# Kernel tuning notes

Hardware: AMD Instinct MI355X
Metric: run time of the kernel (lower is better)

Reference implementation:

```python
import jax, jax.numpy as jnp
import numpy as np

INPUT_DIM = 1024
OUTPUT_DIM = 1024
DEGREE = 8
N_TOKENS = 8192


def setup_inputs() -> dict:
    key = jax.random.key(0)
    k1, k2 = jax.random.split(key)
    x = jax.random.normal(k1, (N_TOKENS, INPUT_DIM), dtype=jnp.float32)
    # xavier_normal_ with gain = 1/(input_dim*(degree+1)) over fan dims (output_dim, degree+1)
    fan_in, fan_out = OUTPUT_DIM, DEGREE + 1  # torch treats dim0/dim1 as fans; scale is tiny anyway
    gain = 1.0 / (INPUT_DIM * (DEGREE + 1))
    std = gain * np.sqrt(2.0 / (INPUT_DIM + OUTPUT_DIM))
    cheby_coeffs = std * jax.random.normal(k2, (INPUT_DIM, OUTPUT_DIM, DEGREE + 1), dtype=jnp.float32)
    return {"x": x, "cheby_coeffs": cheby_coeffs}


def reference(x, cheby_coeffs):
    # x: (..., input_dim) -> y: (..., output_dim)
    degree_p1 = cheby_coeffs.shape[-1]
    theta = jnp.arccos(jnp.tanh(x))                      # (..., i)
    arange = jnp.arange(degree_p1, dtype=x.dtype)        # (d,)
    basis = jnp.cos(theta[..., None] * arange)           # (..., i, d) Chebyshev T_d(tanh(x))
    y = jnp.einsum('...id,iod->...o', basis, cheby_coeffs)
    return y
```

## Files before the change

kernel.cpp:

```cpp
#include <hip/hip_runtime.h>


typedef __bf16 bf16;
typedef __bf16 bf16x8 __attribute__((ext_vector_type(8)));
typedef float f32x2 __attribute__((ext_vector_type(2)));
typedef float f32x4 __attribute__((ext_vector_type(4)));
typedef float f32x16 __attribute__((ext_vector_type(16)));

__device__ __forceinline__ float fast_tanh(float a) {
  float e = __expf(a + a);
  return 1.f - 2.f * __builtin_amdgcn_rcpf(e + 1.f);
}

__global__ __launch_bounds__(256)
void cheby_prep(const float* __restrict__ x, const float* __restrict__ C,
                bf16* __restrict__ Bt, float* __restrict__ bias_p,
                float* __restrict__ th) {
  const int bid = blockIdx.x, tid = threadIdx.x;
  if (bid >= 1024) {
    const int r = bid - 1024;
    f32x4 v = *(const f32x4*)(x + (size_t)r * 1024 + tid * 4);
    f32x4 t;
    #pragma unroll
    for (int j = 0; j < 4; ++j) t[j] = fast_tanh(v[j]);
    *(f32x2*)(th + (size_t)r * 1024 + tid * 2)       = (f32x2){t.x, t.z};
    *(f32x2*)(th + (size_t)r * 1024 + 512 + tid * 2) = (f32x2){t.y, t.w};
    return;
  }
  __shared__ float tile[32][292];
  const int i0 = (bid >> 5) * 32, o0 = (bid & 31) * 32;
  {
    const int r = tid >> 3, seg = tid & 7;
    const float* src = C + (size_t)(i0 + r) * 9216 + (size_t)o0 * 9 + seg * 36;
    float* dst = &tile[r][seg * 36];
    #pragma unroll
    for (int v = 0; v < 9; ++v) *(f32x4*)(dst + v * 4) = *(const f32x4*)(src + v * 4);
  }
  __syncthreads();
  #pragma unroll
  for (int j = 0; j < 4; ++j) {
    int e = tid + 256 * j;
    int il = e >> 5, ol = e & 31;
    int i = i0 + il, o = o0 + ol;
    bf16x8 v;
    #pragma unroll
    for (int d = 0; d < 8; ++d) v[d] = (bf16)tile[il][ol * 9 + 1 + d];
    size_t idx16 = ((size_t)((o >> 7) * 128 + (i >> 3)) * 8 + (i & 7)) * 128 + (o & 127);
    *(bf16x8*)&Bt[idx16 * 8] = v;
  }
  if (tid < 32) {
    float s = 0.f;
    #pragma unroll
    for (int i = 0; i < 32; ++i) s += tile[i][tid * 9];
    bias_p[(size_t)(bid >> 5) * 1024 + o0 + tid] = s;
  }
}

__global__ __launch_bounds__(256, 2)
void cheby_gemm(const float* __restrict__ th, const bf16* __restrict__ Bt,
                const float* __restrict__ bias_p, float* __restrict__ out) {
  const int tid  = threadIdx.x;
  const int lane = tid & 63, w = tid >> 6;
  const int ml = lane & 31, h = lane >> 5;
  const int nb = blockIdx.x & 7;
  const int mb = blockIdx.x >> 3;
  const int wn = w & 1, wm = w >> 1;
  const int t0 = mb * 128 + wm * 64;
  const int o0 = nb * 128 + wn * 64;

  const bf16* btl = Bt + (((size_t)nb * 1024 + h) * 128 + (size_t)wn * 64 + ml) * 8;
  const float* sp0 = th + (size_t)(t0 + ml) * 1024 + h * 512;
  const float* sp1 = sp0 + 32 * 1024;

  f32x16 acc[2][2];
  #pragma unroll
  for (int a = 0; a < 2; ++a)
    #pragma unroll
    for (int b = 0; b < 2; ++b)
      #pragma unroll
      for (int r = 0; r < 16; ++r) acc[a][b][r] = 0.f;

  f32x4  sa[4], sb[4];
  bf16x8 bfr[2][4][2];

  sa[0] = *(const f32x4*)(sp0);     sb[0] = *(const f32x4*)(sp1);
  sa[1] = *(const f32x4*)(sp0 + 4); sb[1] = *(const f32x4*)(sp1 + 4);
  #pragma unroll
  for (int ks = 0; ks < 4; ++ks) {
    bfr[0][ks][0] = *(const bf16x8*)(btl + ks * 2048);
    bfr[0][ks][1] = *(const bf16x8*)(btl + ks * 2048 + 256);
  }

  #pragma unroll 1
  for (int s4 = 0; s4 < 128; s4 += 4) {
    #pragma unroll
    for (int u = 0; u < 4; ++u) {
      const int s = s4 + u;
      {
        int sl = s + 2; if (sl > 127) sl = 127;
        sa[(u + 2) & 3] = *(const f32x4*)(sp0 + sl * 4);
        sb[(u + 2) & 3] = *(const f32x4*)(sp1 + sl * 4);
      }
      {
        int bl = s + 1; if (bl > 127) bl = 127;
        const bf16* g = btl + (size_t)bl * 8192;
        #pragma unroll
        for (int ks = 0; ks < 4; ++ks) {
          bfr[(u + 1) & 1][ks][0] = *(const bf16x8*)(g + ks * 2048);
          bfr[(u + 1) & 1][ks][1] = *(const bf16x8*)(g + ks * 2048 + 256);
        }
      }
      bf16x8 afr[2][4];
      #pragma unroll
      for (int r = 0; r < 2; ++r) {
        const f32x4 sd = r ? sb[u & 3] : sa[u & 3];
        #pragma unroll
        for (int ks = 0; ks < 4; ++ks) {
          const float t  = sd[ks];
          const float T2 = __builtin_fmaf(t + t, t, -1.f);
          const float c2 = T2 + T2;
          const f32x2 c2v = {c2, c2};
          f32x2 pm1 = {t, 1.f};
          f32x2 p   = {t, T2};
          #pragma unroll
          for (int j2 = 0; j2 < 4; ++j2) {
            afr[r][ks][2 * j2]     = (bf16)p.x;
            afr[r][ks][2 * j2 + 1] = (bf16)p.y;
            f32x2 pn = c2v * p - pm1;
            pm1 = p; p = pn;
          }
        }
      }
      #pragma unroll
      for (int ks = 0; ks < 4; ++ks) {
        acc[0][0] = __builtin_amdgcn_mfma_f32_32x32x16_bf16(afr[0][ks], bfr[u & 1][ks][0], acc[0][0], 0, 0, 0);
        acc[0][1] = __builtin_amdgcn_mfma_f32_32x32x16_bf16(afr[0][ks], bfr[u & 1][ks][1], acc[0][1], 0, 0, 0);
        acc[1][0] = __builtin_amdgcn_mfma_f32_32x32x16_bf16(afr[1][ks], bfr[u & 1][ks][0], acc[1][0], 0, 0, 0);
        acc[1][1] = __builtin_amdgcn_mfma_f32_32x32x16_bf16(afr[1][ks], bfr[u & 1][ks][1], acc[1][1], 0, 0, 0);
      }
    }
  }

  float bv0 = 0.f, bv1 = 0.f;
  #pragma unroll
  for (int p = 0; p < 32; ++p) {
    bv0 += bias_p[(size_t)p * 1024 + o0 + ml];
    bv1 += bias_p[(size_t)p * 1024 + o0 + 32 + ml];
  }
  #pragma unroll
  for (int mt = 0; mt < 2; ++mt)
    #pragma unroll
    for (int r = 0; r < 16; ++r) {
      int row = t0 + mt * 32 + (r & 3) + 8 * (r >> 2) + 4 * h;
      float* po = out + (size_t)row * 1024 + o0 + ml;
      po[0]  = acc[mt][0][r] + bv0;
      po[32] = acc[mt][1][r] + bv1;
    }
}

__global__ __launch_bounds__(256)
void cheby_naive(const float* __restrict__ x, const float* __restrict__ C,
                 float* __restrict__ out) {
  const int t = blockIdx.x, tid = threadIdx.x;
  float acc[4] = {0.f, 0.f, 0.f, 0.f};
  for (int i = 0; i < 1024; ++i) {
    float th = tanhf(x[(size_t)t * 1024 + i]);
    float T[9]; T[0] = 1.f; T[1] = th;
    #pragma unroll
    for (int d = 2; d < 9; ++d) T[d] = 2.f * th * T[d - 1] - T[d - 2];
    #pragma unroll
    for (int j = 0; j < 4; ++j) {
      const float* cp = &C[((size_t)i * 1024 + tid + j * 256) * 9];
      float s = 0.f;
      #pragma unroll
      for (int d = 0; d < 9; ++d) s += T[d] * cp[d];
      acc[j] += s;
    }
  }
  #pragma unroll
  for (int j = 0; j < 4; ++j) out[(size_t)t * 1024 + tid + j * 256] = acc[j];
}

extern "C" void kernel_launch(void* const* d_in, const int* in_sizes, int n_in,
                              void* d_out, int out_size, void* d_ws, size_t ws_size,
                              hipStream_t stream) {
  (void)in_sizes; (void)n_in; (void)out_size;
  const float* x = (const float*)d_in[0];
  const float* C = (const float*)d_in[1];
  float* out = (float*)d_out;

  const size_t bt_bytes = (size_t)8 * 128 * 1024 * 8 * sizeof(bf16);
  const size_t bp_bytes = (size_t)32 * 1024 * sizeof(float);
  const size_t th_bytes = (size_t)8192 * 1024 * sizeof(float);

  if (ws_size >= bt_bytes + bp_bytes + th_bytes) {
    bf16*  Bt     = (bf16*)d_ws;
    float* bias_p = (float*)((char*)d_ws + bt_bytes);
    float* th     = (float*)((char*)d_ws + bt_bytes + bp_bytes);
    cheby_prep<<<9216, 256, 0, stream>>>(x, C, Bt, bias_p, th);
    cheby_gemm<<<512, 256, 0, stream>>>(th, Bt, bias_p, out);
  } else {
    cheby_naive<<<8192, 256, 0, stream>>>(x, C, out);
  }
}
```

Baseline: 290.2 us.

## Stage B tiles in LDS via direct global-to-LDS loads and retile GEMM

The GEMM now uses 64x128 output tiles per block (1024 blocks, occupancy 4), with the bf16 B fragments streamed into double-buffered shared memory through global_load_lds and shared by all four waves, instead of each wave loading its own B fragments from global memory. The tanh prep kernel is rewritten to transpose through LDS into an MFMA-fragment-ordered layout, so each lane reads contiguous 32-byte chunks. This cuts redundant B traffic and register pressure, but adds a __syncthreads per k-step and halves the per-wave MFMA work between barriers.

Measured after the change: 301.5 us. +3.9%, slower.

```diff
diff --git a/kernel.cpp b/kernel.cpp
--- a/kernel.cpp
+++ b/kernel.cpp
@@ -7,6 +7,12 @@
 typedef float f32x4 __attribute__((ext_vector_type(4)));
 typedef float f32x16 __attribute__((ext_vector_type(16)));
 
+__device__ __forceinline__ void g2lds16(const void* g, void* l) {
+  __builtin_amdgcn_global_load_lds(
+      (const __attribute__((address_space(1))) unsigned int*)g,
+      (__attribute__((address_space(3))) unsigned int*)l, 16, 0, 0);
+}
+
 __device__ __forceinline__ float fast_tanh(float a) {
   float e = __expf(a + a);
   return 1.f - 2.f * __builtin_amdgcn_rcpf(e + 1.f);
@@ -15,16 +21,41 @@
 __global__ __launch_bounds__(256)
 void cheby_prep(const float* __restrict__ x, const float* __restrict__ C,
                 bf16* __restrict__ Bt, float* __restrict__ bias_p,
-                float* __restrict__ th) {
+                float* __restrict__ thw) {
   const int bid = blockIdx.x, tid = threadIdx.x;
   if (bid >= 1024) {
-    const int r = bid - 1024;
-    f32x4 v = *(const f32x4*)(x + (size_t)r * 1024 + tid * 4);
-    f32x4 t;
-    #pragma unroll
-    for (int j = 0; j < 4; ++j) t[j] = fast_tanh(v[j]);
-    *(f32x2*)(th + (size_t)r * 1024 + tid * 2)       = (f32x2){t.x, t.z};
-    *(f32x2*)(th + (size_t)r * 1024 + 512 + tid * 2) = (f32x2){t.y, t.w};
+    const int b2 = bid - 1024;
+    const int g  = b2 >> 1;
+    const int sh = (b2 & 1) * 64;
+    __shared__ float lt[64][65];
+    for (int c8 = 0; c8 < 8; ++c8) {
+      const int i0 = sh * 8 + c8 * 64;
+      __syncthreads();
+      #pragma unroll
+      for (int p = 0; p < 4; ++p) {
+        int idx = tid + p * 256;
+        int row = idx >> 4, sg = idx & 15;
+        f32x4 v = *(const f32x4*)(x + (size_t)(g * 64 + row) * 1024 + i0 + sg * 4);
+        #pragma unroll
+        for (int j = 0; j < 4; ++j) lt[row][sg * 4 + j] = fast_tanh(v[j]);
+      }
+      __syncthreads();
+      #pragma unroll
+      for (int half = 0; half < 2; ++half) {
+        int slot = tid + half * 256;
+        int js = slot >> 6, ln = slot & 63;
+        int ml = ln & 31, h = ln >> 5;
+        f32x4 v0, v1;
+        #pragma unroll
+        for (int ks = 0; ks < 4; ++ks) {
+          v0[ks] = lt[ml][js * 8 + 2 * ks + h];
+          v1[ks] = lt[32 + ml][js * 8 + 2 * ks + h];
+        }
+        size_t off = ((size_t)(g * 128 + sh + c8 * 8 + js) * 64 + ln) * 8;
+        *(f32x4*)(thw + off)     = v0;
+        *(f32x4*)(thw + off + 4) = v1;
+      }
+    }
     return;
   }
   __shared__ float tile[32][292];
@@ -45,7 +76,7 @@
     bf16x8 v;
     #pragma unroll
     for (int d = 0; d < 8; ++d) v[d] = (bf16)tile[il][ol * 9 + 1 + d];
-    size_t idx16 = ((size_t)((o >> 7) * 128 + (i >> 3)) * 8 + (i & 7)) * 128 + (o & 127);
+    size_t idx16 = (((size_t)(o >> 6) * 128 + (i >> 3)) * 8 + (i & 7)) * 64 + (o & 63);
     *(bf16x8*)&Bt[idx16 * 8] = v;
   }
   if (tid < 32) {
@@ -56,64 +87,55 @@
   }
 }
 
-__global__ __launch_bounds__(256, 2)
-void cheby_gemm(const float* __restrict__ th, const bf16* __restrict__ Bt,
+__global__ __launch_bounds__(256, 4)
+void cheby_gemm(const float* __restrict__ thw, const bf16* __restrict__ Bt,
                 const float* __restrict__ bias_p, float* __restrict__ out) {
+  __shared__ bf16 Bs[2][4096];
+
   const int tid  = threadIdx.x;
   const int lane = tid & 63, w = tid >> 6;
   const int ml = lane & 31, h = lane >> 5;
-  const int nb = blockIdx.x & 7;
-  const int mb = blockIdx.x >> 3;
-  const int wn = w & 1, wm = w >> 1;
-  const int t0 = mb * 128 + wm * 64;
-  const int o0 = nb * 128 + wn * 64;
-
-  const bf16* btl = Bt + (((size_t)nb * 1024 + h) * 128 + (size_t)wn * 64 + ml) * 8;
-  const float* sp0 = th + (size_t)(t0 + ml) * 1024 + h * 512;
-  const float* sp1 = sp0 + 32 * 1024;
-
-  f32x16 acc[2][2];
+  const int wm = w >> 1, wn = w & 1;
+  const int nb = blockIdx.x & 15, mb = blockIdx.x >> 4;
+  const int g  = mb * 2 + wm;
+  const int o0 = nb * 64 + wn * 32;
+
+  const float* sp = thw + ((size_t)g * 128 * 64 + lane) * 8;
+  const bf16* btw = Bt + (((size_t)nb * 128 * 8 + 2 * w) * 64 + lane) * 8;
+
+  f32x16 acc[2];
   #pragma unroll
   for (int a = 0; a < 2; ++a)
     #pragma unroll
-    for (int b = 0; b < 2; ++b)
-      #pragma unroll
-      for (int r = 0; r < 16; ++r) acc[a][b][r] = 0.f;
-
-  f32x4  sa[4], sb[4];
-  bf16x8 bfr[2][4][2];
-
-  sa[0] = *(const f32x4*)(sp0);     sb[0] = *(const f32x4*)(sp1);
-  sa[1] = *(const f32x4*)(sp0 + 4); sb[1] = *(const f32x4*)(sp1 + 4);
-  #pragma unroll
-  for (int ks = 0; ks < 4; ++ks) {
-    bfr[0][ks][0] = *(const bf16x8*)(btl + ks * 2048);
-    bfr[0][ks][1] = *(const bf16x8*)(btl + ks * 2048 + 256);
-  }
+    for (int r = 0; r < 16; ++r) acc[a][r] = 0.f;
+
+  f32x4 sa[4], sb[4];
+
+  sa[0] = *(const f32x4*)(sp);       sb[0] = *(const f32x4*)(sp + 4);
+  sa[1] = *(const f32x4*)(sp + 512); sb[1] = *(const f32x4*)(sp + 516);
+  g2lds16(btw,       &Bs[0][(2 * w) * 512]);
+  g2lds16(btw + 512, &Bs[0][(2 * w + 1) * 512]);
 
   #pragma unroll 1
   for (int s4 = 0; s4 < 128; s4 += 4) {
     #pragma unroll
     for (int u = 0; u < 4; ++u) {
-      const int s = s4 + u;
+      const int s = s4 + u, bi = u & 1;
+      __syncthreads();
+      if (s < 127) {
+        const bf16* gsrc = btw + (size_t)(s + 1) * 4096;
+        g2lds16(gsrc,       &Bs[bi ^ 1][(2 * w) * 512]);
+        g2lds16(gsrc + 512, &Bs[bi ^ 1][(2 * w + 1) * 512]);
+      }
       {
-        int sl = s + 2; if (sl > 127) sl = 127;
-        sa[(u + 2) & 3] = *(const f32x4*)(sp0 + sl * 4);
-        sb[(u + 2) & 3] = *(const f32x4*)(sp1 + sl * 4);
-      }
-      {
-        int bl = s + 1; if (bl > 127) bl = 127;
-        const bf16* g = btl + (size_t)bl * 8192;
-        #pragma unroll
-        for (int ks = 0; ks < 4; ++ks) {
-          bfr[(u + 1) & 1][ks][0] = *(const bf16x8*)(g + ks * 2048);
-          bfr[(u + 1) & 1][ks][1] = *(const bf16x8*)(g + ks * 2048 + 256);
-        }
+        const int sl = (s + 2 < 127) ? s + 2 : 127;
+        sa[(u + 2) & 3] = *(const f32x4*)(sp + (size_t)sl * 512);
+        sb[(u + 2) & 3] = *(const f32x4*)(sp + (size_t)sl * 512 + 4);
       }
       bf16x8 afr[2][4];
       #pragma unroll
       for (int r = 0; r < 2; ++r) {
-        const f32x4 sd = r ? sb[u & 3] : sa[u & 3];
+        const f32x4 sd = r ? sb[u] : sa[u];
         #pragma unroll
         for (int ks = 0; ks < 4; ++ks) {
           const float t  = sd[ks];
@@ -133,29 +155,25 @@
       }
       #pragma unroll
       for (int ks = 0; ks < 4; ++ks) {
-        acc[0][0] = __builtin_amdgcn_mfma_f32_32x32x16_bf16(afr[0][ks], bfr[u & 1][ks][0], acc[0][0], 0, 0, 0);
-        acc[0][1] = __builtin_amdgcn_mfma_f32_32x32x16_bf16(afr[0][ks], bfr[u & 1][ks][1], acc[0][1], 0, 0, 0);
-        acc[1][0] = __builtin_amdgcn_mfma_f32_32x32x16_bf16(afr[1][ks], bfr[u & 1][ks][0], acc[1][0], 0, 0, 0);
-        acc[1][1] = __builtin_amdgcn_mfma_f32_32x32x16_bf16(afr[1][ks], bfr[u & 1][ks][1], acc[1][1], 0, 0, 0);
-      }
-    }
-  }
-
-  float bv0 = 0.f, bv1 = 0.f;
-  #pragma unroll
-  for (int p = 0; p < 32; ++p) {
-    bv0 += bias_p[(size_t)p * 1024 + o0 + ml];
-    bv1 += bias_p[(size_t)p * 1024 + o0 + 32 + ml];
-  }
+        bf16x8 bf = *(const bf16x8*)&Bs[bi][((ks * 2 + h) * 64 + wn * 32 + ml) * 8];
+        acc[0] = __builtin_amdgcn_mfma_f32_32x32x16_bf16(afr[0][ks], bf, acc[0], 0, 0, 0);
+        acc[1] = __builtin_amdgcn_mfma_f32_32x32x16_bf16(afr[1][ks], bf, acc[1], 0, 0, 0);
+      }
+    }
+  }
+
+  const int c0 = nb * 64 + wn * 32 + ml;
+  float bv = 0.f;
+  #pragma unroll
+  for (int p = 0; p < 32; ++p) bv += bias_p[(size_t)p * 1024 + c0];
   #pragma unroll
   for (int mt = 0; mt < 2; ++mt)
     #pragma unroll
     for (int r = 0; r < 16; ++r) {
-      int row = t0 + mt * 32 + (r & 3) + 8 * (r >> 2) + 4 * h;
-      float* po = out + (size_t)row * 1024 + o0 + ml;
-      po[0]  = acc[mt][0][r] + bv0;
-      po[32] = acc[mt][1][r] + bv1;
-    }
+      int row = g * 64 + mt * 32 + (r & 3) + 8 * (r >> 2) + 4 * h;
+      out[(size_t)row * 1024 + c0] = acc[mt][r] + bv;
+    }
+  (void)o0;
 }
 
 __global__ __launch_bounds__(256)
@@ -189,16 +207,16 @@
   const float* C = (const float*)d_in[1];
   float* out = (float*)d_out;
 
-  const size_t bt_bytes = (size_t)8 * 128 * 1024 * 8 * sizeof(bf16);
+  const size_t bt_bytes = (size_t)1024 * 8192 * sizeof(bf16);
   const size_t bp_bytes = (size_t)32 * 1024 * sizeof(float);
   const size_t th_bytes = (size_t)8192 * 1024 * sizeof(float);
 
   if (ws_size >= bt_bytes + bp_bytes + th_bytes) {
     bf16*  Bt     = (bf16*)d_ws;
     float* bias_p = (float*)((char*)d_ws + bt_bytes);
-    float* th     = (float*)((char*)d_ws + bt_bytes + bp_bytes);
-    cheby_prep<<<9216, 256, 0, stream>>>(x, C, Bt, bias_p, th);
-    cheby_gemm<<<512, 256, 0, stream>>>(th, Bt, bias_p, out);
+    float* thw    = (float*)((char*)d_ws + bt_bytes + bp_bytes);
+    cheby_prep<<<1280, 256, 0, stream>>>(x, C, Bt, bias_p, thw);
+    cheby_gemm<<<1024, 256, 0, stream>>>(thw, Bt, bias_p, out);
   } else {
     cheby_naive<<<8192, 256, 0, stream>>>(x, C, out);
   }
```
